# Kernel tuning notes

Measured on AMD Instinct MI355X. Metric: run time of the kernel, lower is better.

Reference implementation:

```python
import jax, jax.numpy as jnp
import numpy as np

EPSILON = 0.0

def setup_inputs() -> dict:
    key = jax.random.key(0)
    k1, k2, k3, k4, k5 = jax.random.split(key, 5)
    N, MAX_NB, D_IN, D_OUT, N_BONDS = 50000, 16, 256, 256, 400000
    x = jax.random.normal(k1, (N, D_IN), dtype=jnp.float32)
    W = jax.random.normal(k2, (D_OUT, D_IN), dtype=jnp.float32) * (1.0 / np.sqrt(D_IN))
    b = jax.random.normal(k3, (D_OUT,), dtype=jnp.float32) * 0.01
    b_from_a = jax.random.randint(k4, (N_BONDS,), 0, N, dtype=jnp.int32)
    a_from_b = jax.random.randint(k5, (N, MAX_NB), 0, N_BONDS, dtype=jnp.int32)
    return {"x": x, "W": W, "b": b, "b_from_a": b_from_a, "a_from_b": a_from_b}

def reference(x, W, b, b_from_a, a_from_b):
    # a2a[i, k] = source atom of the k-th neighbor bond of atom i
    a2a = b_from_a[a_from_b]                      # [N, max_nb]
    h = x @ W.T + b                               # [N, d_out]
    h = h.at[0].set(0.0)                          # row 0 is padding
    message = h[a2a]                              # [N, max_nb, d_out] gather
    out = (1.0 + EPSILON) * h + jnp.sum(message, axis=1)
    return jax.nn.relu(out)
```

## Files before the change

kernel.cpp:

```cpp
#include <hip/hip_runtime.h>

typedef short bf16x8 __attribute__((ext_vector_type(8)));
typedef float f32x4  __attribute__((ext_vector_type(4)));

__device__ __forceinline__ unsigned short f32_to_bf16(float f) {
  union { float f; unsigned int u; } v; v.f = f;
  unsigned int u = v.u;
  u += 0x7fffu + ((u >> 16) & 1u);
  return (unsigned short)(u >> 16);
}
__device__ __forceinline__ float bf16lo_to_f32(unsigned int u) {
  union { unsigned int u; float f; } v; v.u = u << 16; return v.f;
}
__device__ __forceinline__ float bf16hi_to_f32(unsigned int u) {
  union { unsigned int u; float f; } v; v.u = u & 0xffff0000u; return v.f;
}

#define LDSTRIDE 40

__global__ __launch_bounds__(256, 2) void gin_gemm(
    const float* __restrict__ x, const float* __restrict__ W,
    const float* __restrict__ bias, unsigned short* __restrict__ h, int M) {
  __shared__ __align__(16) unsigned short Xs[128 * LDSTRIDE];
  __shared__ __align__(16) unsigned short Ws[128 * LDSTRIDE];

  const int tid  = threadIdx.x;
  const int wid  = tid >> 6;
  const int lane = tid & 63;
  const int row0  = blockIdx.x * 128;
  const int ncol0 = blockIdx.y * 128;

  f32x4 acc[2][8] = {};

  const int srow = tid >> 2;
  const int sk0  = (tid & 3) << 3;
  int ar0 = row0 + srow;        if (ar0 >= M) ar0 = M - 1;
  int ar1 = row0 + 64 + srow;   if (ar1 >= M) ar1 = M - 1;
  const float* aRow0 = x + (size_t)ar0 * 256 + sk0;
  const float* aRow1 = x + (size_t)ar1 * 256 + sk0;
  const float* bRow0 = W + (size_t)(ncol0 + srow) * 256 + sk0;
  const float* bRow1 = W + (size_t)(ncol0 + 64 + srow) * 256 + sk0;

  const int quad = lane >> 4;
  const int c16  = lane & 15;
  float4 biasv[2];
#pragma unroll
  for (int ng = 0; ng < 2; ++ng)
    biasv[ng] = *(const float4*)(bias + ncol0 + wid * 32 + ng * 16 + quad * 4);

  for (int kt = 0; kt < 8; ++kt) {
    const int kb = kt * 32;
#pragma unroll
    for (int p = 0; p < 2; ++p) {
      const float* src = p ? aRow1 : aRow0;
      float4 v0 = *(const float4*)(src + kb);
      float4 v1 = *(const float4*)(src + kb + 4);
      bf16x8 u;
      u[0] = (short)f32_to_bf16(v0.x); u[1] = (short)f32_to_bf16(v0.y);
      u[2] = (short)f32_to_bf16(v0.z); u[3] = (short)f32_to_bf16(v0.w);
      u[4] = (short)f32_to_bf16(v1.x); u[5] = (short)f32_to_bf16(v1.y);
      u[6] = (short)f32_to_bf16(v1.z); u[7] = (short)f32_to_bf16(v1.w);
      *(bf16x8*)(&Xs[(p * 64 + srow) * LDSTRIDE + sk0]) = u;
    }
#pragma unroll
    for (int p = 0; p < 2; ++p) {
      const float* src = p ? bRow1 : bRow0;
      float4 v0 = *(const float4*)(src + kb);
      float4 v1 = *(const float4*)(src + kb + 4);
      bf16x8 u;
      u[0] = (short)f32_to_bf16(v0.x); u[1] = (short)f32_to_bf16(v0.y);
      u[2] = (short)f32_to_bf16(v0.z); u[3] = (short)f32_to_bf16(v0.w);
      u[4] = (short)f32_to_bf16(v1.x); u[5] = (short)f32_to_bf16(v1.y);
      u[6] = (short)f32_to_bf16(v1.z); u[7] = (short)f32_to_bf16(v1.w);
      *(bf16x8*)(&Ws[(p * 64 + srow) * LDSTRIDE + sk0]) = u;
    }
    __syncthreads();

    const int r16 = lane & 15;
    const int qk  = (lane >> 4) << 3;
    bf16x8 wf[2], xf[8];
#pragma unroll
    for (int g = 0; g < 2; ++g)
      wf[g] = *(const bf16x8*)(&Ws[(wid * 32 + g * 16 + r16) * LDSTRIDE + qk]);
#pragma unroll
    for (int g = 0; g < 8; ++g)
      xf[g] = *(const bf16x8*)(&Xs[(g * 16 + r16) * LDSTRIDE + qk]);
#pragma unroll
    for (int ng = 0; ng < 2; ++ng)
#pragma unroll
      for (int ag = 0; ag < 8; ++ag)
        acc[ng][ag] = __builtin_amdgcn_mfma_f32_16x16x32_bf16(
            wf[ng], xf[ag], acc[ng][ag], 0, 0, 0);
    __syncthreads();
  }

#pragma unroll
  for (int ag = 0; ag < 8; ++ag) {
    const int atom = row0 + ag * 16 + c16;
    if (atom >= M) continue;
#pragma unroll
    for (int ng = 0; ng < 2; ++ng) {
      const int n0 = ncol0 + wid * 32 + ng * 16 + quad * 4;
      float v0 = acc[ng][ag][0] + biasv[ng].x;
      float v1 = acc[ng][ag][1] + biasv[ng].y;
      float v2 = acc[ng][ag][2] + biasv[ng].z;
      float v3 = acc[ng][ag][3] + biasv[ng].w;
      if (atom == 0) { v0 = v1 = v2 = v3 = 0.0f; }
      uint2 pk;
      pk.x = (unsigned int)f32_to_bf16(v0) | ((unsigned int)f32_to_bf16(v1) << 16);
      pk.y = (unsigned int)f32_to_bf16(v2) | ((unsigned int)f32_to_bf16(v3) << 16);
      *(uint2*)(h + (size_t)atom * 256 + n0) = pk;
    }
  }
}

__global__ __launch_bounds__(256, 4) void gin_gather(
    const unsigned short* __restrict__ h, const int* __restrict__ b_from_a,
    const int* __restrict__ a_from_b, float* __restrict__ out, int N) {
  const int wid  = threadIdx.x >> 6;
  const int lane = threadIdx.x & 63;
  const int i = blockIdx.x * 4 + wid;
  if (i >= N) return;

  const int half = lane >> 5;
  const int hl   = lane & 31;
  const int c0   = hl << 3;

  int src = 0;
  if (lane < 16) src = b_from_a[a_from_b[i * 16 + lane]];

  const unsigned short* hp = h + c0;

  int s[8];
#pragma unroll
  for (int k = 0; k < 8; ++k) s[k] = __shfl(src, half * 8 + k, 64);

  uint4 vself = *(const uint4*)(hp + (size_t)i * 256);
  uint4 v[8];
#pragma unroll
  for (int k = 0; k < 8; ++k)
    v[k] = *(const uint4*)(hp + (size_t)s[k] * 256);

  const float selfw = half ? 0.0f : 1.0f;
  float a0 = selfw * bf16lo_to_f32(vself.x), a1 = selfw * bf16hi_to_f32(vself.x);
  float a2 = selfw * bf16lo_to_f32(vself.y), a3 = selfw * bf16hi_to_f32(vself.y);
  float a4 = selfw * bf16lo_to_f32(vself.z), a5 = selfw * bf16hi_to_f32(vself.z);
  float a6 = selfw * bf16lo_to_f32(vself.w), a7 = selfw * bf16hi_to_f32(vself.w);
#pragma unroll
  for (int k = 0; k < 8; ++k) {
    a0 += bf16lo_to_f32(v[k].x); a1 += bf16hi_to_f32(v[k].x);
    a2 += bf16lo_to_f32(v[k].y); a3 += bf16hi_to_f32(v[k].y);
    a4 += bf16lo_to_f32(v[k].z); a5 += bf16hi_to_f32(v[k].z);
    a6 += bf16lo_to_f32(v[k].w); a7 += bf16hi_to_f32(v[k].w);
  }
  a0 += __shfl_xor(a0, 32, 64); a1 += __shfl_xor(a1, 32, 64);
  a2 += __shfl_xor(a2, 32, 64); a3 += __shfl_xor(a3, 32, 64);
  a4 += __shfl_xor(a4, 32, 64); a5 += __shfl_xor(a5, 32, 64);
  a6 += __shfl_xor(a6, 32, 64); a7 += __shfl_xor(a7, 32, 64);

  float4 r;
  if (half == 0) {
    r.x = fmaxf(a0, 0.0f); r.y = fmaxf(a1, 0.0f);
    r.z = fmaxf(a2, 0.0f); r.w = fmaxf(a3, 0.0f);
  } else {
    r.x = fmaxf(a4, 0.0f); r.y = fmaxf(a5, 0.0f);
    r.z = fmaxf(a6, 0.0f); r.w = fmaxf(a7, 0.0f);
  }
  *(float4*)(out + (size_t)i * 256 + c0 + half * 4) = r;
}

extern "C" void kernel_launch(void* const* d_in, const int* in_sizes, int n_in,
                              void* d_out, int out_size, void* d_ws, size_t ws_size,
                              hipStream_t stream) {
  const float* x        = (const float*)d_in[0];
  const float* W        = (const float*)d_in[1];
  const float* b        = (const float*)d_in[2];
  const int*   b_from_a = (const int*)d_in[3];
  const int*   a_from_b = (const int*)d_in[4];
  float*       out      = (float*)d_out;
  const int M = in_sizes[0] / 256;

  unsigned short* h = (unsigned short*)d_ws;

  dim3 ggrid((M + 127) / 128, 2);
  gin_gemm<<<ggrid, 256, 0, stream>>>(x, W, b, h, M);
  gin_gather<<<(M + 3) / 4, 256, 0, stream>>>(h, b_from_a, a_from_b, out, M);
}
```

Baseline: 202.1 us.

## Restructure gather into 64-atom by 32-column tiles with LDS-staged neighbor indices

```diff
diff --git a/kernel.cpp b/kernel.cpp
--- a/kernel.cpp
+++ b/kernel.cpp
@@ -117,56 +117,64 @@
 __global__ __launch_bounds__(256, 4) void gin_gather(
     const unsigned short* __restrict__ h, const int* __restrict__ b_from_a,
     const int* __restrict__ a_from_b, float* __restrict__ out, int N) {
+  __shared__ int srcs[64 * 17];
+
+  const int chunk = blockIdx.x & 7;
+  const int atom0 = (blockIdx.x >> 3) * 64;
+
+  {
+    const int t = threadIdx.x;
+    int g0 = atom0 * 16 + t * 4;
+    int4 bonds;
+    if (g0 + 3 < N * 16) {
+      bonds = *(const int4*)(a_from_b + g0);
+    } else {
+      bonds.x = bonds.y = bonds.z = bonds.w = 0;
+    }
+    const int la = t >> 2;
+    const int k0 = (t & 3) * 4;
+    srcs[la * 17 + k0 + 0] = b_from_a[bonds.x];
+    srcs[la * 17 + k0 + 1] = b_from_a[bonds.y];
+    srcs[la * 17 + k0 + 2] = b_from_a[bonds.z];
+    srcs[la * 17 + k0 + 3] = b_from_a[bonds.w];
+  }
+  __syncthreads();
+
   const int wid  = threadIdx.x >> 6;
   const int lane = threadIdx.x & 63;
-  const int i = blockIdx.x * 4 + wid;
-  if (i >= N) return;
+  const int la   = wid * 16 + (lane >> 2);
+  const int atom = atom0 + la;
+  if (atom >= N) return;
 
-  const int half = lane >> 5;
-  const int hl   = lane & 31;
-  const int c0   = hl << 3;
+  const int col = chunk * 32 + (lane & 3) * 8;
+  const unsigned short* hp = h + col;
 
-  int src = 0;
-  if (lane < 16) src = b_from_a[a_from_b[i * 16 + lane]];
+  int s[16];
+#pragma unroll
+  for (int k = 0; k < 16; ++k) s[k] = srcs[la * 17 + k];
 
-  const unsigned short* hp = h + c0;
+  uint4 v = *(const uint4*)(hp + (size_t)atom * 256);
+  float a0 = bf16lo_to_f32(v.x), a1 = bf16hi_to_f32(v.x);
+  float a2 = bf16lo_to_f32(v.y), a3 = bf16hi_to_f32(v.y);
+  float a4 = bf16lo_to_f32(v.z), a5 = bf16hi_to_f32(v.z);
+  float a6 = bf16lo_to_f32(v.w), a7 = bf16hi_to_f32(v.w);
+#pragma unroll
+  for (int k = 0; k < 16; ++k) {
+    uint4 w = *(const uint4*)(hp + (size_t)s[k] * 256);
+    a0 += bf16lo_to_f32(w.x); a1 += bf16hi_to_f32(w.x);
+    a2 += bf16lo_to_f32(w.y); a3 += bf16hi_to_f32(w.y);
+    a4 += bf16lo_to_f32(w.z); a5 += bf16hi_to_f32(w.z);
+    a6 += bf16lo_to_f32(w.w); a7 += bf16hi_to_f32(w.w);
+  }
 
-  int s[8];
-#pragma unroll
-  for (int k = 0; k < 8; ++k) s[k] = __shfl(src, half * 8 + k, 64);
-
-  uint4 vself = *(const uint4*)(hp + (size_t)i * 256);
-  uint4 v[8];
-#pragma unroll
-  for (int k = 0; k < 8; ++k)
-    v[k] = *(const uint4*)(hp + (size_t)s[k] * 256);
-
-  const float selfw = half ? 0.0f : 1.0f;
-  float a0 = selfw * bf16lo_to_f32(vself.x), a1 = selfw * bf16hi_to_f32(vself.x);
-  float a2 = selfw * bf16lo_to_f32(vself.y), a3 = selfw * bf16hi_to_f32(vself.y);
-  float a4 = selfw * bf16lo_to_f32(vself.z), a5 = selfw * bf16hi_to_f32(vself.z);
-  float a6 = selfw * bf16lo_to_f32(vself.w), a7 = selfw * bf16hi_to_f32(vself.w);
-#pragma unroll
-  for (int k = 0; k < 8; ++k) {
-    a0 += bf16lo_to_f32(v[k].x); a1 += bf16hi_to_f32(v[k].x);
-    a2 += bf16lo_to_f32(v[k].y); a3 += bf16hi_to_f32(v[k].y);
-    a4 += bf16lo_to_f32(v[k].z); a5 += bf16hi_to_f32(v[k].z);
-    a6 += bf16lo_to_f32(v[k].w); a7 += bf16hi_to_f32(v[k].w);
-  }
-  a0 += __shfl_xor(a0, 32, 64); a1 += __shfl_xor(a1, 32, 64);
-  a2 += __shfl_xor(a2, 32, 64); a3 += __shfl_xor(a3, 32, 64);
-  a4 += __shfl_xor(a4, 32, 64); a5 += __shfl_xor(a5, 32, 64);
-  a6 += __shfl_xor(a6, 32, 64); a7 += __shfl_xor(a7, 32, 64);
-
-  float4 r;
-  if (half == 0) {
-    r.x = fmaxf(a0, 0.0f); r.y = fmaxf(a1, 0.0f);
-    r.z = fmaxf(a2, 0.0f); r.w = fmaxf(a3, 0.0f);
-  } else {
-    r.x = fmaxf(a4, 0.0f); r.y = fmaxf(a5, 0.0f);
-    r.z = fmaxf(a6, 0.0f); r.w = fmaxf(a7, 0.0f);
-  }
-  *(float4*)(out + (size_t)i * 256 + c0 + half * 4) = r;
+  float* op = out + (size_t)atom * 256 + col;
+  float4 r0, r1;
+  r0.x = fmaxf(a0, 0.0f); r0.y = fmaxf(a1, 0.0f);
+  r0.z = fmaxf(a2, 0.0f); r0.w = fmaxf(a3, 0.0f);
+  r1.x = fmaxf(a4, 0.0f); r1.y = fmaxf(a5, 0.0f);
+  r1.z = fmaxf(a6, 0.0f); r1.w = fmaxf(a7, 0.0f);
+  *(float4*)(op)     = r0;
+  *(float4*)(op + 4) = r1;
 }
 
 extern "C" void kernel_launch(void* const* d_in, const int* in_sizes, int n_in,
@@ -184,5 +192,6 @@
 
   dim3 ggrid((M + 127) / 128, 2);
   gin_gemm<<<ggrid, 256, 0, stream>>>(x, W, b, h, M);
-  gin_gather<<<(M + 3) / 4, 256, 0, stream>>>(h, b_from_a, a_from_b, out, M);
+  const int ablocks = (M + 63) / 64;
+  gin_gather<<<ablocks * 8, 256, 0, stream>>>(h, b_from_a, a_from_b, out, M);
 }
```

After: 232.1 us. +14.8%, slower.
